# Performance work log

Measured on AMD Instinct MI355X. Metric: run time of the kernel, lower is better.

Reference implementation:

```python
import jax, jax.numpy as jnp
import numpy as np
from jax.scipy.special import logsumexp

B = 2048       # anchors
P = 4          # positives per anchor (constant -> ragged list collapses to [B,P])
D = 256        # embed dim
N_NEG = 32768  # shared negative bank
TEMPERATURE = 0.05
ALPHA = 0.1
EPS = 1e-12    # F.normalize eps


def _l2norm(x):
    n = jnp.sqrt(jnp.sum(x * x, axis=-1, keepdims=True))
    return x / jnp.maximum(n, EPS)


def setup_inputs() -> dict:
    key = jax.random.key(0)
    k1, k2, k3 = jax.random.split(key, 3)
    return {
        "anchor_embeddings": jax.random.normal(k1, (B, D), jnp.float32),
        "positive_embeddings": jax.random.normal(k2, (B * P, D), jnp.float32),
        "negative_embeddings": jax.random.normal(k3, (N_NEG, D), jnp.float32),
        "num_positives_per_anchor": jnp.full((B,), P, dtype=jnp.int32),
    }


def reference(anchor_embeddings, positive_embeddings, negative_embeddings,
              num_positives_per_anchor):
    a = _l2norm(anchor_embeddings)                       # [B, D]
    p = _l2norm(positive_embeddings).reshape(B, P, D)    # [B, P, D]
    n = _l2norm(negative_embeddings)                     # [N, D]

    pos_sim = jnp.einsum("bd,bpd->bp", a, p) / TEMPERATURE   # [B, P]
    neg_sim = jnp.einsum("bd,nd->bn", a, n) / TEMPERATURE    # [B, N]  (dominant traffic)
    neg_lse = logsumexp(neg_sim, axis=1)                     # [B]

    # per-(anchor, positive) CE with label 0 over logits [pos_j, neg_sim_i]:
    # loss = logsumexp([pos_j, neg...]) - pos_j = logaddexp(pos_j, neg_lse_i) - pos_j
    pair_loss = jnp.logaddexp(pos_sim, neg_lse[:, None]) - pos_sim   # [B, P]
    counts = num_positives_per_anchor
    pair_mask = jnp.arange(P)[None, :] < counts[:, None]             # [B, P]
    total = jnp.sum(jnp.where(pair_mask, pair_loss, 0.0))

    # weighted-positive term (only for anchors with num_pos > 1)
    w = jax.nn.softmax(pos_sim, axis=1)                  # [B, P]
    wps = jnp.sum(w * pos_sim, axis=1)                   # [B]
    wloss = jnp.logaddexp(wps, neg_lse) - wps            # [B]
    total = total + ALPHA * jnp.sum(jnp.where(counts > 1, wloss, 0.0))

    return total / B
```

## Files before the change

### kernel.cpp

```cpp
#include <hip/hip_runtime.h>
#include <math.h>

constexpr int   B       = 2048;
constexpr int   P       = 4;
constexpr int   D       = 256;
constexpr int   NNEG    = 32768;
constexpr int   NTILES  = NNEG / 64;
constexpr float TEMP    = 0.05f;
constexpr float ALPHA   = 0.1f;
constexpr float EPS     = 1e-12f;
constexpr float INV_T   = 1.0f / TEMP;
constexpr float SCALE_Q = 28.853900817779268f;

typedef float f32x4 __attribute__((ext_vector_type(4)));
typedef int   i32x8 __attribute__((ext_vector_type(8)));

__device__ inline unsigned short f2bf(float f) {
  unsigned int u = __float_as_uint(f);
  u = (u + 0x7fffu + ((u >> 16) & 1u)) >> 16;
  return (unsigned short)u;
}
__device__ inline float bf2f(unsigned short u) {
  return __uint_as_float((unsigned int)u << 16);
}


constexpr int NPANEL = (B + NNEG) / 16;
constexpr int LSTR   = 264;

__global__ __launch_bounds__(256) void prep_kernel(
    const float* __restrict__ a,
    const float* __restrict__ pzx,
    const float* __restrict__ n,
    unsigned char* __restrict__ a_f8,
    unsigned char* __restrict__ n_f8,
    float* __restrict__ pos_sim,
    float* __restrict__ loss_acc,
    unsigned int* __restrict__ ticket) {
  if (blockIdx.x == 0 && threadIdx.x == 0) { *loss_acc = 0.0f; *ticket = 0u; }
  const int id   = blockIdx.x;
  const int tid  = threadIdx.x;
  const int wave = tid >> 6;
  const int lane = tid & 63;

  if (id < NPANEL) {
    __shared__ __align__(16) unsigned short sm[16 * LSTR];
    const float* src; unsigned char* dst; int prow; float post;
    if (id < B / 16) { src = a; dst = a_f8; prow = id;          post = SCALE_Q; }
    else             { src = n; dst = n_f8; prow = id - B / 16; post = 1.0f; }

#pragma unroll
    for (int rr = 0; rr < 4; rr++) {
      const int r = wave * 4 + rr;
      float4 v = ((const float4*)(src + ((size_t)prow * 16 + r) * D))[lane];
      float ss = v.x * v.x + v.y * v.y + v.z * v.z + v.w * v.w;
#pragma unroll
      for (int off = 32; off > 0; off >>= 1) ss += __shfl_xor(ss, off, 64);
      float inv = post / fmaxf(sqrtf(ss), EPS);
      ushort4 o;
      o.x = f2bf(v.x * inv); o.y = f2bf(v.y * inv);
      o.z = f2bf(v.z * inv); o.w = f2bf(v.w * inv);
      *(ushort4*)&sm[r * LSTR + lane * 4] = o;
    }
    __syncthreads();

    const int r1 = (2 * tid) & 15;
    const int r2 = (2 * tid + 1) & 15;
    const int k0 = (tid >> 5) * 32 + ((tid >> 3) & 3) * 8;
    const unsigned short* s1 = &sm[r1 * LSTR + k0];
    const unsigned short* s2 = &sm[r2 * LSTR + k0];
    uint4 ov;
    {
      int w0 = __builtin_amdgcn_cvt_pk_fp8_f32(bf2f(s1[0]), bf2f(s1[1]), 0, false);
      w0     = __builtin_amdgcn_cvt_pk_fp8_f32(bf2f(s1[2]), bf2f(s1[3]), w0, true);
      int w1 = __builtin_amdgcn_cvt_pk_fp8_f32(bf2f(s1[4]), bf2f(s1[5]), 0, false);
      w1     = __builtin_amdgcn_cvt_pk_fp8_f32(bf2f(s1[6]), bf2f(s1[7]), w1, true);
      int w2 = __builtin_amdgcn_cvt_pk_fp8_f32(bf2f(s2[0]), bf2f(s2[1]), 0, false);
      w2     = __builtin_amdgcn_cvt_pk_fp8_f32(bf2f(s2[2]), bf2f(s2[3]), w2, true);
      int w3 = __builtin_amdgcn_cvt_pk_fp8_f32(bf2f(s2[4]), bf2f(s2[5]), 0, false);
      w3     = __builtin_amdgcn_cvt_pk_fp8_f32(bf2f(s2[6]), bf2f(s2[7]), w3, true);
      ov.x = (unsigned)w0; ov.y = (unsigned)w1;
      ov.z = (unsigned)w2; ov.w = (unsigned)w3;
    }
    *(uint4*)(dst + (size_t)prow * 4096 + tid * 16) = ov;
  } else {
    int pw = (id - NPANEL) * 4 + wave;
    if (pw >= B * P) return;
    int b = pw >> 2;
    float4 av = ((const float4*)(a + (size_t)b * D))[lane];
    float4 pv = ((const float4*)(pzx + (size_t)pw * D))[lane];
    float d  = av.x * pv.x + av.y * pv.y + av.z * pv.z + av.w * pv.w;
    float sa = av.x * av.x + av.y * av.y + av.z * av.z + av.w * av.w;
    float sp = pv.x * pv.x + pv.y * pv.y + pv.z * pv.z + pv.w * pv.w;
#pragma unroll
    for (int off = 32; off > 0; off >>= 1) {
      d  += __shfl_xor(d, off, 64);
      sa += __shfl_xor(sa, off, 64);
      sp += __shfl_xor(sp, off, 64);
    }
    if (lane == 0) {
      float inva = 1.0f / fmaxf(sqrtf(sa), EPS);
      float invp = 1.0f / fmaxf(sqrtf(sp), EPS);
      pos_sim[pw] = d * inva * invp * INV_T;
    }
  }
}

constexpr int BM = 64, BN = 256;

__global__ __launch_bounds__(512, 4) void negsim_mfma_kernel(
    const unsigned char* __restrict__ Af,
    const unsigned char* __restrict__ Nf,
    float* __restrict__ part_s) {
  __shared__ __align__(16) unsigned char As[32 * 512];
  __shared__ float part_l[8][64];

  const int tid  = threadIdx.x;
  const int wave = tid >> 6;
  const int lane = tid & 63;

  const int id   = blockIdx.x;
  const int xcd  = id & 7;
  const int j    = id >> 3;
  const int nblk = xcd * 16 + (j & 15);
  const int mblk = j >> 4;
  const int m0   = mblk * BM;
  const int n0   = nblk * BN;

#pragma unroll
  for (int t = 0; t < 2; t++) {
    const int s = wave * 2 + t;
    __builtin_amdgcn_global_load_lds(
        (const __attribute__((address_space(1))) unsigned int*)
            (Af + (size_t)(m0 >> 4) * 4096 + s * 1024 + lane * 16),
        (__attribute__((address_space(3))) unsigned int*)(As + s * 1024 + lane * 16),
        16, 0, 0);
  }

  const unsigned char* Bp = Nf + (size_t)((n0 >> 4) + wave * 2) * 4096 + lane * 8;

  i32x8 bf0[2], bf1[2];
#pragma unroll
  for (int ni = 0; ni < 2; ni++) {
#pragma unroll
    for (int q = 0; q < 4; q++) {
      int2 v = *(const int2*)(Bp + (size_t)ni * 4096 + q * 512);
      bf0[ni][2 * q]     = v.x;
      bf0[ni][2 * q + 1] = v.y;
    }
#pragma unroll
    for (int q = 0; q < 4; q++) {
      int2 v = *(const int2*)(Bp + (size_t)ni * 4096 + (4 + q) * 512);
      bf1[ni][2 * q]     = v.x;
      bf1[ni][2 * q + 1] = v.y;
    }
  }

  __syncthreads();

  f32x4 acc[4][2] = {};

  {
    i32x8 af[4];
#pragma unroll
    for (int mi = 0; mi < 4; mi++)
#pragma unroll
      for (int q = 0; q < 4; q++) {
        int2 v = *(const int2*)&As[(mi * 8 + q) * 512 + lane * 8];
        af[mi][2 * q]     = v.x;
        af[mi][2 * q + 1] = v.y;
      }
#pragma unroll
    for (int mi = 0; mi < 4; mi++)
#pragma unroll
      for (int ni = 0; ni < 2; ni++)
        acc[mi][ni] = __builtin_amdgcn_mfma_scale_f32_16x16x128_f8f6f4(
            af[mi], bf0[ni], acc[mi][ni],
            0, 0,
            0, 0x7f7f7f7f,
            0, 0x7f7f7f7f);
  }

  {
    i32x8 af[4];
#pragma unroll
    for (int mi = 0; mi < 4; mi++)
#pragma unroll
      for (int q = 0; q < 4; q++) {
        int2 v = *(const int2*)&As[(mi * 8 + 4 + q) * 512 + lane * 8];
        af[mi][2 * q]     = v.x;
        af[mi][2 * q + 1] = v.y;
      }
#pragma unroll
    for (int mi = 0; mi < 4; mi++)
#pragma unroll
      for (int ni = 0; ni < 2; ni++)
        acc[mi][ni] = __builtin_amdgcn_mfma_scale_f32_16x16x128_f8f6f4(
            af[mi], bf1[ni], acc[mi][ni],
            0, 0,
            0, 0x7f7f7f7f,
            0, 0x7f7f7f7f);
  }

#pragma unroll
  for (int mi = 0; mi < 4; mi++) {
#pragma unroll
    for (int rr = 0; rr < 4; rr++) {
      float s = __builtin_amdgcn_exp2f(acc[mi][0][rr]) +
                __builtin_amdgcn_exp2f(acc[mi][1][rr]);
#pragma unroll
      for (int off = 1; off < 16; off <<= 1) s += __shfl_xor(s, off, 64);
      if ((lane & 15) == 0)
        part_l[wave][mi * 16 + (lane >> 4) * 4 + rr] = s;
    }
  }
  __syncthreads();
  if (tid < 256) {
    const int u   = tid >> 6;
    const int row = tid & 63;
    float s64 = part_l[2 * u][row] + part_l[2 * u + 1][row];
    part_s[(size_t)(m0 + row) * NTILES + (nblk * 4 + u)] = s64;
  }
}

__global__ void loss_kernel(const float* __restrict__ part_s,
                            const float* __restrict__ pos_sim,
                            const int* __restrict__ counts,
                            float* __restrict__ loss_acc,
                            unsigned int* __restrict__ ticket,
                            float* __restrict__ out) {
  const int tid = threadIdx.x;
  const int b   = blockIdx.x * 16 + (tid >> 4);
  const int sub = tid & 15;
  const float* ps = part_s + (size_t)b * NTILES;
  float s = 0.0f;
#pragma unroll
  for (int i = 0; i < NTILES / 16; i++) s += ps[sub + i * 16];
  s += __shfl_xor(s, 1, 64);
  s += __shfl_xor(s, 2, 64);
  s += __shfl_xor(s, 4, 64);
  s += __shfl_xor(s, 8, 64);

  float acc = 0.0f;
  if (sub == 0) {
    float L = logf(s);
    float p0 = pos_sim[b * P + 0], p1 = pos_sim[b * P + 1];
    float p2 = pos_sim[b * P + 2], p3 = pos_sim[b * P + 3];
    int cnt = counts[b];
    float pj[P] = {p0, p1, p2, p3};
#pragma unroll
    for (int jj = 0; jj < P; jj++) {
      if (jj < cnt) {
        float hi = fmaxf(pj[jj], L), lo = fminf(pj[jj], L);
        acc += hi + log1pf(__expf(lo - hi)) - pj[jj];
      }
    }
    float mp = fmaxf(fmaxf(p0, p1), fmaxf(p2, p3));
    float e0 = __expf(p0 - mp), e1 = __expf(p1 - mp);
    float e2 = __expf(p2 - mp), e3 = __expf(p3 - mp);
    float se = e0 + e1 + e2 + e3;
    float wps = (e0 * p0 + e1 * p1 + e2 * p2 + e3 * p3) / se;
    if (cnt > 1) {
      float hi = fmaxf(wps, L), lo = fminf(wps, L);
      acc += ALPHA * (hi + log1pf(__expf(lo - hi)) - wps);
    }
  }
#pragma unroll
  for (int off = 32; off > 0; off >>= 1) acc += __shfl_xor(acc, off, 64);
  __shared__ float sa[4];
  int wid = tid >> 6, lane = tid & 63;
  if (lane == 0) sa[wid] = acc;
  __syncthreads();
  if (tid == 0) {
    atomicAdd(loss_acc, sa[0] + sa[1] + sa[2] + sa[3]);
    __threadfence();
    unsigned int t = atomicAdd(ticket, 1u);
    if (t == (unsigned int)gridDim.x - 1u) {
      float total = atomicAdd(loss_acc, 0.0f);
      out[0] = total / (float)B;
    }
  }
}

extern "C" void kernel_launch(void* const* d_in, const int* in_sizes, int n_in,
                              void* d_out, int out_size, void* d_ws,
                              size_t ws_size, hipStream_t stream) {
  const float* anc    = (const float*)d_in[0];
  const float* pos    = (const float*)d_in[1];
  const float* neg    = (const float*)d_in[2];
  const int*   counts = (const int*)d_in[3];
  float* out = (float*)d_out;

  unsigned char* a_f8 = (unsigned char*)d_ws;
  unsigned char* n_f8 = a_f8 + (size_t)B * D;
  float* part_s  = (float*)(n_f8 + (size_t)NNEG * D);
  float* pos_sim = part_s + (size_t)B * NTILES;
  float* loss_acc = pos_sim + B * P;
  unsigned int* ticket = (unsigned int*)(loss_acc + 1);

  prep_kernel<<<NPANEL + B * P / 4, 256, 0, stream>>>(
      anc, pos, neg, a_f8, n_f8, pos_sim, loss_acc, ticket);

  negsim_mfma_kernel<<<4096, 512, 0, stream>>>(a_f8, n_f8, part_s);

  loss_kernel<<<B / 16, 256, 0, stream>>>(part_s, pos_sim, counts,
                                          loss_acc, ticket, out);
}
```

Before: 143.1 us.

## Repack FP8 operands for 32-byte fragment loads and use DPP row reductions

The prep kernel now writes each 16-row FP8 panel so that every lane's 32-byte MFMA operand fragment (16 elements from one row per 16-byte chunk) is contiguous. This lets the GEMM kernel fetch the A and B fragments with single 32-byte vector loads instead of many 8-byte loads. The 16-lane shuffle reduction of exp sums is also replaced by DPP row-rotate adds, avoiding cross-lane shuffles. The risk is that the new layout must match the MFMA K-ordering on both operands, and the ror-based reduction gives the full sum in every lane.

```diff
diff --git a/kernel.cpp b/kernel.cpp
--- a/kernel.cpp
+++ b/kernel.cpp
@@ -22,6 +22,19 @@
 }
 __device__ inline float bf2f(unsigned short u) {
   return __uint_as_float((unsigned int)u << 16);
+}
+
+__device__ inline float ror16_add(float v) {
+  int x;
+  x = __builtin_amdgcn_update_dpp(0, __float_as_int(v), 0x121, 0xf, 0xf, true);
+  v += __int_as_float(x);
+  x = __builtin_amdgcn_update_dpp(0, __float_as_int(v), 0x122, 0xf, 0xf, true);
+  v += __int_as_float(x);
+  x = __builtin_amdgcn_update_dpp(0, __float_as_int(v), 0x124, 0xf, 0xf, true);
+  v += __int_as_float(x);
+  x = __builtin_amdgcn_update_dpp(0, __float_as_int(v), 0x128, 0xf, 0xf, true);
+  v += __int_as_float(x);
+  return v;
 }
 
 
@@ -64,21 +77,20 @@
     }
     __syncthreads();
 
-    const int r1 = (2 * tid) & 15;
-    const int r2 = (2 * tid + 1) & 15;
-    const int k0 = (tid >> 5) * 32 + ((tid >> 3) & 3) * 8;
-    const unsigned short* s1 = &sm[r1 * LSTR + k0];
-    const unsigned short* s2 = &sm[r2 * LSTR + k0];
+    const int o  = tid * 16;
+    const int r  = (o >> 5) & 15;
+    const int k0 = (o >> 11) * 128 + ((o >> 9) & 3) * 32 + (o & 31);
+    const unsigned short* s1 = &sm[r * LSTR + k0];
     uint4 ov;
     {
-      int w0 = __builtin_amdgcn_cvt_pk_fp8_f32(bf2f(s1[0]), bf2f(s1[1]), 0, false);
-      w0     = __builtin_amdgcn_cvt_pk_fp8_f32(bf2f(s1[2]), bf2f(s1[3]), w0, true);
-      int w1 = __builtin_amdgcn_cvt_pk_fp8_f32(bf2f(s1[4]), bf2f(s1[5]), 0, false);
-      w1     = __builtin_amdgcn_cvt_pk_fp8_f32(bf2f(s1[6]), bf2f(s1[7]), w1, true);
-      int w2 = __builtin_amdgcn_cvt_pk_fp8_f32(bf2f(s2[0]), bf2f(s2[1]), 0, false);
-      w2     = __builtin_amdgcn_cvt_pk_fp8_f32(bf2f(s2[2]), bf2f(s2[3]), w2, true);
-      int w3 = __builtin_amdgcn_cvt_pk_fp8_f32(bf2f(s2[4]), bf2f(s2[5]), 0, false);
-      w3     = __builtin_amdgcn_cvt_pk_fp8_f32(bf2f(s2[6]), bf2f(s2[7]), w3, true);
+      int w0 = __builtin_amdgcn_cvt_pk_fp8_f32(bf2f(s1[0]),  bf2f(s1[1]),  0,  false);
+      w0     = __builtin_amdgcn_cvt_pk_fp8_f32(bf2f(s1[2]),  bf2f(s1[3]),  w0, true);
+      int w1 = __builtin_amdgcn_cvt_pk_fp8_f32(bf2f(s1[4]),  bf2f(s1[5]),  0,  false);
+      w1     = __builtin_amdgcn_cvt_pk_fp8_f32(bf2f(s1[6]),  bf2f(s1[7]),  w1, true);
+      int w2 = __builtin_amdgcn_cvt_pk_fp8_f32(bf2f(s1[8]),  bf2f(s1[9]),  0,  false);
+      w2     = __builtin_amdgcn_cvt_pk_fp8_f32(bf2f(s1[10]), bf2f(s1[11]), w2, true);
+      int w3 = __builtin_amdgcn_cvt_pk_fp8_f32(bf2f(s1[12]), bf2f(s1[13]), 0,  false);
+      w3     = __builtin_amdgcn_cvt_pk_fp8_f32(bf2f(s1[14]), bf2f(s1[15]), w3, true);
       ov.x = (unsigned)w0; ov.y = (unsigned)w1;
       ov.z = (unsigned)w2; ov.w = (unsigned)w3;
     }
@@ -112,7 +124,7 @@
     const unsigned char* __restrict__ Af,
     const unsigned char* __restrict__ Nf,
     float* __restrict__ part_s) {
-  __shared__ __align__(16) unsigned char As[32 * 512];
+  __shared__ __align__(16) unsigned char As[4 * 4096];
   __shared__ float part_l[8][64];
 
   const int tid  = threadIdx.x;
@@ -137,81 +149,43 @@
         16, 0, 0);
   }
 
-  const unsigned char* Bp = Nf + (size_t)((n0 >> 4) + wave * 2) * 4096 + lane * 8;
-
-  i32x8 bf0[2], bf1[2];
-#pragma unroll
-  for (int ni = 0; ni < 2; ni++) {
-#pragma unroll
-    for (int q = 0; q < 4; q++) {
-      int2 v = *(const int2*)(Bp + (size_t)ni * 4096 + q * 512);
-      bf0[ni][2 * q]     = v.x;
-      bf0[ni][2 * q + 1] = v.y;
-    }
-#pragma unroll
-    for (int q = 0; q < 4; q++) {
-      int2 v = *(const int2*)(Bp + (size_t)ni * 4096 + (4 + q) * 512);
-      bf1[ni][2 * q]     = v.x;
-      bf1[ni][2 * q + 1] = v.y;
-    }
-  }
+  const unsigned char* Bp = Nf + (size_t)((n0 >> 4) + wave * 2) * 4096 + lane * 32;
+
+  i32x8 bf[2][2];
+#pragma unroll
+  for (int ni = 0; ni < 2; ni++)
+#pragma unroll
+    for (int h = 0; h < 2; h++)
+      bf[ni][h] = *(const i32x8*)(Bp + (size_t)ni * 4096 + h * 2048);
 
   __syncthreads();
 
   f32x4 acc[4][2] = {};
 
-  {
-    i32x8 af[4];
-#pragma unroll
-    for (int mi = 0; mi < 4; mi++)
-#pragma unroll
-      for (int q = 0; q < 4; q++) {
-        int2 v = *(const int2*)&As[(mi * 8 + q) * 512 + lane * 8];
-        af[mi][2 * q]     = v.x;
-        af[mi][2 * q + 1] = v.y;
-      }
-#pragma unroll
-    for (int mi = 0; mi < 4; mi++)
+#pragma unroll
+  for (int h = 0; h < 2; h++) {
+#pragma unroll
+    for (int mi = 0; mi < 4; mi++) {
+      i32x8 af = *(const i32x8*)&As[mi * 4096 + h * 2048 + lane * 32];
 #pragma unroll
       for (int ni = 0; ni < 2; ni++)
         acc[mi][ni] = __builtin_amdgcn_mfma_scale_f32_16x16x128_f8f6f4(
-            af[mi], bf0[ni], acc[mi][ni],
+            af, bf[ni][h], acc[mi][ni],
             0, 0,
             0, 0x7f7f7f7f,
             0, 0x7f7f7f7f);
-  }
-
-  {
-    i32x8 af[4];
-#pragma unroll
-    for (int mi = 0; mi < 4; mi++)
-#pragma unroll
-      for (int q = 0; q < 4; q++) {
-        int2 v = *(const int2*)&As[(mi * 8 + 4 + q) * 512 + lane * 8];
-        af[mi][2 * q]     = v.x;
-        af[mi][2 * q + 1] = v.y;
-      }
-#pragma unroll
-    for (int mi = 0; mi < 4; mi++)
-#pragma unroll
-      for (int ni = 0; ni < 2; ni++)
-        acc[mi][ni] = __builtin_amdgcn_mfma_scale_f32_16x16x128_f8f6f4(
-            af[mi], bf1[ni], acc[mi][ni],
-            0, 0,
-            0, 0x7f7f7f7f,
-            0, 0x7f7f7f7f);
+    }
   }
 
 #pragma unroll
   for (int mi = 0; mi < 4; mi++) {
 #pragma unroll
     for (int rr = 0; rr < 4; rr++) {
-      float s = __builtin_amdgcn_exp2f(acc[mi][0][rr]) +
+      float e = __builtin_amdgcn_exp2f(acc[mi][0][rr]) +
                 __builtin_amdgcn_exp2f(acc[mi][1][rr]);
-#pragma unroll
-      for (int off = 1; off < 16; off <<= 1) s += __shfl_xor(s, off, 64);
+      e = ror16_add(e);
       if ((lane & 15) == 0)
-        part_l[wave][mi * 16 + (lane >> 4) * 4 + rr] = s;
+        part_l[wave][mi * 16 + (lane >> 4) * 4 + rr] = e;
     }
   }
   __syncthreads();
```

Result: faster. 121.3 us (-15.3%).
